# Optimization experiments

Hardware: AMD Instinct MI355X
Metric: run time of the kernel (lower is better)

Reference implementation:

```python
import jax, jax.numpy as jnp
import numpy as np

B, S, HID, NH, HD, NL = 2, 4096, 1024, 16, 64, 128
N_ITER = 6


def setup_inputs() -> dict:
    key = jax.random.key(0)
    ks = jax.random.split(key, 9)
    s = 0.02
    D = NH * HD
    return {
        "X": jax.random.normal(ks[0], (B, S, HID), jnp.float32),
        "mask": jnp.ones((B, S), jnp.float32),
        "Wq": jax.random.normal(ks[1], (HID, D), jnp.float32) * s,
        "bq": jnp.zeros((D,), jnp.float32),
        "Wk": jax.random.normal(ks[2], (HID, D), jnp.float32) * s,
        "bk": jnp.zeros((D,), jnp.float32),
        "Wv": jax.random.normal(ks[3], (HID, D), jnp.float32) * s,
        "bv": jnp.zeros((D,), jnp.float32),
        "Wo": jax.random.normal(ks[4], (D, HID), jnp.float32) * s,
        "bo": jnp.zeros((HID,), jnp.float32),
    }


def iterative_inv(mat, n_iter=N_ITER):
    # Newton-Schulz style pseudo-inverse iteration (Nystromformer 'original' init)
    I = jnp.eye(mat.shape[-1], dtype=mat.dtype)
    K = mat
    V = K.swapaxes(-1, -2) / jnp.max(jnp.sum(K, axis=-2))
    for _ in range(n_iter):
        KV = K @ V
        V = 0.25 * V @ (13.0 * I - KV @ (15.0 * I - KV @ (7.0 * I - KV)))
    return V


def nystrom_core(Q, K, V, mask):
    # Q,K,V: [B,NH,S,HD], mask: [B,S]
    scale = 1.0 / np.sqrt(np.sqrt(HD))  # 1/d^(1/4) applied to both Q and K
    m = mask[:, None, :, None]
    Q = Q * m * scale
    K = K * m * scale
    seg = S // NL
    # landmarks: mean over contiguous segments -> [B,NH,NL,HD]
    Ql = Q.reshape(B, NH, NL, seg, HD).mean(axis=-2)
    Kl = K.reshape(B, NH, NL, seg, HD).mean(axis=-2)
    k1 = jax.nn.softmax(jnp.einsum('bhsd,bhld->bhsl', Q, Kl), axis=-1)   # [B,NH,S,NL]
    k2 = jax.nn.softmax(jnp.einsum('bhld,bhmd->bhlm', Ql, Kl), axis=-1)  # [B,NH,NL,NL]
    k3 = jax.nn.softmax(
        jnp.einsum('bhld,bhsd->bhls', Ql, K) - 1e9 * (1.0 - mask[:, None, None, :]),
        axis=-1)                                                          # [B,NH,NL,S]
    return k1 @ iterative_inv(k2) @ (k3 @ V)                              # [B,NH,S,HD]


def reference(X, mask, Wq, bq, Wk, bk, Wv, bv, Wo, bo):
    def split(Y):  # [B,S,NH*HD] -> [B,NH,S,HD]
        return Y.reshape(B, S, NH, HD).transpose(0, 2, 1, 3)
    Q = split(X @ Wq + bq)
    K = split(X @ Wk + bk)
    V = split(X @ Wv + bv)
    attn = nystrom_core(Q.astype(jnp.float32), K.astype(jnp.float32),
                        V.astype(jnp.float32), mask.astype(jnp.float32))
    out = attn.transpose(0, 2, 1, 3).reshape(B, S, NH * HD)
    return out @ Wo + bo
```

## Files before the change

### kernel.cpp

```cpp
#include <hip/hip_runtime.h>
#include <math.h>

constexpr int cB = 2, cS = 4096, cHID = 1024, cNH = 16, cHD = 64, cNL = 128, cSEG = 32, cD = 1024, cBH = 32;
constexpr float cSCALE = 0.35355339059327373f;

typedef _Float16 f16x8 __attribute__((ext_vector_type(8)));
typedef float f32x4 __attribute__((ext_vector_type(4)));

__device__ inline void gload_lds16(const void* g, void* l) {
    __builtin_amdgcn_global_load_lds(
        (const __attribute__((address_space(1))) void*)g,
        (__attribute__((address_space(3))) void*)l, 16, 0, 0);
}

__global__ __launch_bounds__(256) void wcast_t(
    const float* __restrict__ Wq, const float* __restrict__ Wk,
    const float* __restrict__ Wv, const float* __restrict__ Wo,
    _Float16* __restrict__ WqT, _Float16* __restrict__ WkT,
    _Float16* __restrict__ WvT, _Float16* __restrict__ WoT)
{
    __shared__ float tile[32][33];
    const int wsel = blockIdx.z;
    const float* W = (wsel == 0) ? Wq : (wsel == 1 ? Wk : (wsel == 2 ? Wv : Wo));
    _Float16* WT   = (wsel == 0) ? WqT : (wsel == 1 ? WkT : (wsel == 2 ? WvT : WoT));
    const int n0 = blockIdx.x * 32, k0 = blockIdx.y * 32;
    const int t = threadIdx.x;
    const int r = t >> 3, c = (t & 7) * 4;
    float4 v = *reinterpret_cast<const float4*>(W + (size_t)(k0 + r) * cD + n0 + c);
    tile[r][c] = v.x; tile[r][c + 1] = v.y; tile[r][c + 2] = v.z; tile[r][c + 3] = v.w;
    __syncthreads();
    union { _Float16 h[4]; ushort4 u; } p;
    p.h[0] = (_Float16)tile[c + 0][r]; p.h[1] = (_Float16)tile[c + 1][r];
    p.h[2] = (_Float16)tile[c + 2][r]; p.h[3] = (_Float16)tile[c + 3][r];
    *reinterpret_cast<ushort4*>(WT + (size_t)(n0 + r) * cHID + k0 + c) = p.u;
}

__global__ __launch_bounds__(64) void xm_kernel(
    const float* __restrict__ X, const float* __restrict__ mask,
    float* __restrict__ Xm, float* __restrict__ mbar, _Float16* __restrict__ Xh)
{
    const int bl = blockIdx.x;
    const int q  = blockIdx.y;
    const int b = bl >> 7, l = bl & 127;
    const int c = q * 256 + threadIdx.x * 4;
    float4 a = {0.f, 0.f, 0.f, 0.f};
    float msum = 0.f;
    for (int j = 0; j < cSEG; ++j) {
        float m = mask[b * cS + l * cSEG + j];
        size_t roff = ((size_t)(b * cS + l * cSEG + j)) * cHID + c;
        float4 x = *reinterpret_cast<const float4*>(X + roff);
        union { _Float16 h[4]; ushort4 u; } p;
        p.h[0] = (_Float16)x.x; p.h[1] = (_Float16)x.y;
        p.h[2] = (_Float16)x.z; p.h[3] = (_Float16)x.w;
        *reinterpret_cast<ushort4*>(Xh + roff) = p.u;
        a.x += m * x.x; a.y += m * x.y; a.z += m * x.z; a.w += m * x.w;
        msum += m;
    }
    const float inv = 1.0f / cSEG;
    a.x *= inv; a.y *= inv; a.z *= inv; a.w *= inv;
    *reinterpret_cast<float4*>(Xm + (size_t)bl * cHID + c) = a;
    if (q == 0 && threadIdx.x == 0) mbar[bl] = msum * inv;
}

__global__ __launch_bounds__(256) void qkv_gemm_f16(
    const _Float16* __restrict__ Xh, const float* __restrict__ mask,
    const _Float16* __restrict__ WqT, const _Float16* __restrict__ WkT, const _Float16* __restrict__ WvT,
    const float* __restrict__ bq, const float* __restrict__ bk, const float* __restrict__ bv,
    _Float16* __restrict__ Qh, _Float16* __restrict__ Kh, _Float16* __restrict__ Vh)
{
    __shared__ __align__(16) _Float16 As[128 * 64];
    __shared__ __align__(16) _Float16 Bs[128 * 64];
    const int wsel = blockIdx.z;
    const _Float16* WT = (wsel == 0) ? WqT : (wsel == 1 ? WkT : WvT);
    const float* bias  = (wsel == 0) ? bq  : (wsel == 1 ? bk  : bv);
    _Float16* Y        = (wsel == 0) ? Qh  : (wsel == 1 ? Kh  : Vh);
    const int orig = blockIdx.x;
    const int xcd = orig & 7, idx = orig >> 3;
    const int n0 = (idx & 7) * 128;
    const int m0 = (xcd * 8 + (idx >> 3)) * 128;
    const int t = threadIdx.x;
    const int wave = t >> 6, lane = t & 63;
    const int wm = (wave >> 1) * 64, wn = (wave & 1) * 64;
    const int quad = lane >> 4, l15 = lane & 15;
    const int srow = wave * 8 + (lane >> 3);
    const int scol = ((lane & 7) ^ (lane >> 3)) * 8;

    f32x4 acc[4][4];
#pragma unroll
    for (int i = 0; i < 4; ++i)
#pragma unroll
        for (int j = 0; j < 4; ++j) acc[i][j] = (f32x4){0.f, 0.f, 0.f, 0.f};

    for (int k0 = 0; k0 < cHID; k0 += 64) {
        const _Float16* aSrc = Xh + (size_t)(m0 + srow) * cHID + k0 + scol;
        const _Float16* bSrc = WT + (size_t)(n0 + srow) * cHID + k0 + scol;
#pragma unroll
        for (int i = 0; i < 4; ++i) {
            gload_lds16(aSrc + (size_t)(i * 32) * cHID, &As[(wave * 8 + i * 32) * 64]);
            gload_lds16(bSrc + (size_t)(i * 32) * cHID, &Bs[(wave * 8 + i * 32) * 64]);
        }
        __syncthreads();
        f16x8 af[2][4], bf[2][4];
#pragma unroll
        for (int kh = 0; kh < 2; ++kh) {
            const int cg = ((kh * 4 + quad) ^ (l15 & 7)) * 8;
#pragma unroll
            for (int mt = 0; mt < 4; ++mt)
                af[kh][mt] = *reinterpret_cast<const f16x8*>(&As[(wm + mt * 16 + l15) * 64 + cg]);
#pragma unroll
            for (int nt = 0; nt < 4; ++nt)
                bf[kh][nt] = *reinterpret_cast<const f16x8*>(&Bs[(wn + nt * 16 + l15) * 64 + cg]);
        }
#pragma unroll
        for (int kh = 0; kh < 2; ++kh)
#pragma unroll
            for (int mt = 0; mt < 4; ++mt)
#pragma unroll
                for (int nt = 0; nt < 4; ++nt)
                    acc[mt][nt] = __builtin_amdgcn_mfma_f32_16x16x32_f16(af[kh][mt], bf[kh][nt], acc[mt][nt], 0, 0, 0);
        __syncthreads();
    }
#pragma unroll
    for (int mt = 0; mt < 4; ++mt) {
#pragma unroll
        for (int r = 0; r < 4; ++r) {
            int R = m0 + wm + mt * 16 + quad * 4 + r;
            int b = R >> 12, s = R & (cS - 1);
            float msc = (wsel < 2) ? mask[b * cS + s] * cSCALE : 1.0f;
#pragma unroll
            for (int nt = 0; nt < 4; ++nt) {
                int Cc = n0 + wn + nt * 16 + l15;
                int h = Cc >> 6, d = Cc & 63;
                float val = (acc[mt][nt][r] + bias[Cc]) * msc;
                Y[((size_t)(b * cNH + h) * cS + s) * cHD + d] = (_Float16)val;
            }
        }
    }
}

__global__ __launch_bounds__(256) void out_gemm_f16(
    const _Float16* __restrict__ Ah, const _Float16* __restrict__ WT,
    const float* __restrict__ bias, float* __restrict__ Y)
{
    __shared__ __align__(16) _Float16 As[128 * 64];
    __shared__ __align__(16) _Float16 Bs[128 * 64];
    const int orig = blockIdx.x;
    const int xcd = orig & 7, idx = orig >> 3;
    const int n0 = (idx & 7) * 128;
    const int m0 = (xcd * 8 + (idx >> 3)) * 128;
    const int t = threadIdx.x;
    const int wave = t >> 6, lane = t & 63;
    const int wm = (wave >> 1) * 64, wn = (wave & 1) * 64;
    const int quad = lane >> 4, l15 = lane & 15;
    const int srow = wave * 8 + (lane >> 3);
    const int scol = ((lane & 7) ^ (lane >> 3)) * 8;

    f32x4 acc[4][4];
#pragma unroll
    for (int i = 0; i < 4; ++i)
#pragma unroll
        for (int j = 0; j < 4; ++j) acc[i][j] = (f32x4){0.f, 0.f, 0.f, 0.f};

    for (int k0 = 0; k0 < cD; k0 += 64) {
        const _Float16* aSrc = Ah + (size_t)(m0 + srow) * cD + k0 + scol;
        const _Float16* bSrc = WT + (size_t)(n0 + srow) * cD + k0 + scol;
#pragma unroll
        for (int i = 0; i < 4; ++i) {
            gload_lds16(aSrc + (size_t)(i * 32) * cD, &As[(wave * 8 + i * 32) * 64]);
            gload_lds16(bSrc + (size_t)(i * 32) * cD, &Bs[(wave * 8 + i * 32) * 64]);
        }
        __syncthreads();
        f16x8 af[2][4], bf[2][4];
#pragma unroll
        for (int kh = 0; kh < 2; ++kh) {
            const int cg = ((kh * 4 + quad) ^ (l15 & 7)) * 8;
#pragma unroll
            for (int mt = 0; mt < 4; ++mt)
                af[kh][mt] = *reinterpret_cast<const f16x8*>(&As[(wm + mt * 16 + l15) * 64 + cg]);
#pragma unroll
            for (int nt = 0; nt < 4; ++nt)
                bf[kh][nt] = *reinterpret_cast<const f16x8*>(&Bs[(wn + nt * 16 + l15) * 64 + cg]);
        }
#pragma unroll
        for (int kh = 0; kh < 2; ++kh)
#pragma unroll
            for (int mt = 0; mt < 4; ++mt)
#pragma unroll
                for (int nt = 0; nt < 4; ++nt)
                    acc[mt][nt] = __builtin_amdgcn_mfma_f32_16x16x32_f16(af[kh][mt], bf[kh][nt], acc[mt][nt], 0, 0, 0);
        __syncthreads();
    }
#pragma unroll
    for (int mt = 0; mt < 4; ++mt) {
#pragma unroll
        for (int r = 0; r < 4; ++r) {
            int R = m0 + wm + mt * 16 + quad * 4 + r;
#pragma unroll
            for (int nt = 0; nt < 4; ++nt) {
                int Cc = n0 + wn + nt * 16 + l15;
                Y[(size_t)R * cHID + Cc] = acc[mt][nt][r] + bias[Cc];
            }
        }
    }
}

__global__ __launch_bounds__(256) void lgemm(
    const float* __restrict__ Xm, const float* __restrict__ mbar,
    const float* __restrict__ Wq, const float* __restrict__ bq,
    const float* __restrict__ Wk, const float* __restrict__ bk,
    float* __restrict__ Ql, float* __restrict__ Kl,
    _Float16* __restrict__ Qlh, _Float16* __restrict__ Klh)
{
    __shared__ __align__(16) float As[16][68];
    __shared__ __align__(16) float Bs[16][68];
    const int tid = threadIdx.x;
    const int wsel = blockIdx.z;
    const float* W    = wsel ? Wk : Wq;
    const float* bias = wsel ? bk : bq;
    float* Yl         = wsel ? Kl : Ql;
    _Float16* Ylh     = wsel ? Klh : Qlh;
// ... 40 lines not shown
}

__global__ __launch_bounds__(128) void k2_softmax(
    const float* __restrict__ Ql, const float* __restrict__ Kl, float* __restrict__ k2)
{
    __shared__ __align__(16) float qrow[64];
    __shared__ float red[128];
    int bh = blockIdx.x >> 7, i = blockIdx.x & 127;
    int j = threadIdx.x;
    if (j < 64) qrow[j] = Ql[(bh * cNL + i) * cHD + j];
    __syncthreads();
    const float4* q4  = reinterpret_cast<const float4*>(qrow);
    const float4* kl4 = reinterpret_cast<const float4*>(Kl + (bh * cNL + j) * cHD);
    float dot = 0.f;
#pragma unroll
    for (int u = 0; u < 16; ++u) {
        float4 a = q4[u], b = kl4[u];
        dot += a.x * b.x + a.y * b.y + a.z * b.z + a.w * b.w;
    }
    red[j] = dot; __syncthreads();
    for (int off = 64; off > 0; off >>= 1) { if (j < off) red[j] = fmaxf(red[j], red[j + off]); __syncthreads(); }
    float m = red[0]; __syncthreads();
    float e = expf(dot - m);
    red[j] = e; __syncthreads();
    for (int off = 64; off > 0; off >>= 1) { if (j < off) red[j] += red[j + off]; __syncthreads(); }
    k2[(bh * cNL + i) * cNL + j] = e / red[0];
}

__global__ __launch_bounds__(128) void colsum_max(const float* __restrict__ k2, int* __restrict__ cmax)
{
    __shared__ float red[128];
    int bh = blockIdx.x, j = threadIdx.x;
    float s = 0.f;
    for (int i = 0; i < cNL; ++i) s += k2[(bh * cNL + i) * cNL + j];
    red[j] = s; __syncthreads();
    for (int off = 64; off > 0; off >>= 1) { if (j < off) red[j] = fmaxf(red[j], red[j + off]); __syncthreads(); }
    if (j == 0) atomicMax(cmax, __float_as_int(red[0]));
}

__device__ inline void split2(float v, _Float16& h, _Float16& l) {
    h = (_Float16)v;
    l = (_Float16)(v - (float)h);
}
__device__ inline unsigned short f16bits(_Float16 h) { return __builtin_bit_cast(unsigned short, h); }

#define NYS_MFMA(a, b, c) __builtin_amdgcn_mfma_f32_16x16x32_f16((a), (b), (c), 0, 0, 0)

#define NYS_PRELOAD(PH, PL, LH, LL)                                                     \
    {                                                                                   \
        _Pragma("unroll")                                                               \
        for (int mt_ = 0; mt_ < 4; ++mt_) {                                             \
            const int rowL_ = wr * 64 + mt_ * 16 + l15;                                 \
            _Pragma("unroll")                                                           \
            for (int k0_ = 0; k0_ < 4; ++k0_) {                                         \
                LH[mt_][k0_] = *reinterpret_cast<const f16x8*>(&PH[rowL_ * 136 + k0_ * 32 + quad * 8]); \
                LL[mt_][k0_] = *reinterpret_cast<const f16x8*>(&PL[rowL_ * 136 + k0_ * 32 + quad * 8]); \
            }                                                                           \
        }                                                                               \
    }

#define NYS_PRODUCT(PH, PL, LH, LL)                                                     \
    {                                                                                   \
        _Pragma("unroll")                                                               \
        for (int mt_ = 0; mt_ < 4; ++mt_)                                               \
            _Pragma("unroll")                                                           \
            for (int nt_ = 0; nt_ < 2; ++nt_) acc[mt_][nt_] = (f32x4){0.f, 0.f, 0.f, 0.f}; \
        _Pragma("unroll")                                                               \
        for (int nt_ = 0; nt_ < 2; ++nt_) {                                             \
            _Pragma("unroll")                                                           \
            for (int k0_ = 0; k0_ < 4; ++k0_) {                                         \
                const int boff_ = (wcb + nt_ * 16) * 136 + k0_ * 32 + quad * 8;         \
                f16x8 bh_ = *reinterpret_cast<const f16x8*>(&PH[boff_]);                \
                f16x8 bl_ = *reinterpret_cast<const f16x8*>(&PL[boff_]);                \
                _Pragma("unroll")                                                       \
                for (int mt_ = 0; mt_ < 4; ++mt_) {                                     \
                    acc[mt_][nt_] = NYS_MFMA(LH[mt_][k0_], bh_, acc[mt_][nt_]);         \
                    acc[mt_][nt_] = NYS_MFMA(LL[mt_][k0_], bh_, acc[mt_][nt_]);         \
                    acc[mt_][nt_] = NYS_MFMA(LH[mt_][k0_], bl_, acc[mt_][nt_]);         \
                }                                                                       \
            }                                                                           \
        }                                                                               \
    }

__global__ __launch_bounds__(512, 2) void nys_k3v(
    const float* __restrict__ k2, const int* __restrict__ cmax,
    float* __restrict__ Mg0, float* __restrict__ Mg1,
    const _Float16* __restrict__ Qlh, const _Float16* __restrict__ Kh,
    const _Float16* __restrict__ VTh, const float* __restrict__ mask,
    float* __restrict__ Opart, float* __restrict__ mpart, float* __restrict__ spart)
{
    __shared__ __align__(16) _Float16 SMEM[4 * 128 * 136];

    if (blockIdx.x < 32) {
        _Float16* Ahi_s = SMEM;
        _Float16* Alo_s = SMEM + 128 * 136;
        _Float16* Whi_s = SMEM + 2 * 128 * 136;
        _Float16* Wlo_s = SMEM + 3 * 128 * 136;
        const int bh = blockIdx.x;
        const int t = threadIdx.x;
        const int wave = t >> 6, lane = t & 63;
        const int wr = wave >> 2, wc = wave & 3;
        const int quad = lane >> 4, l15 = lane & 15;
        const int wcb = wc * 32 + l15;
        const float* Kg = k2 + (size_t)bh * 16384;
        float* Mg0b = Mg0 + (size_t)bh * 16384;
        float* Mg1b = Mg1 + (size_t)bh * 16384;
        const float sc = sqrtf(1.0f / __int_as_float(*cmax));

        {
            const int row = t >> 2, c0 = (t & 3) * 32;
            const float* src = Kg + row * 128 + c0;
            _Float16* dh = &Whi_s[row * 136 + c0];
            _Float16* dl = &Wlo_s[row * 136 + c0];
#pragma unroll
            for (int u = 0; u < 32; u += 4) {
                float4 v = *reinterpret_cast<const float4*>(src + u);
                ushort4 ph, pl; _Float16 h, l;
                split2(v.x * sc, h, l); ph.x = f16bits(h); pl.x = f16bits(l);
                split2(v.y * sc, h, l); ph.y = f16bits(h); pl.y = f16bits(l);
                split2(v.z * sc, h, l); ph.z = f16bits(h); pl.z = f16bits(l);
                split2(v.w * sc, h, l); ph.w = f16bits(h); pl.w = f16bits(l);
                *reinterpret_cast<ushort4*>(dh + u) = ph;
                *reinterpret_cast<ushort4*>(dl + u) = pl;
            }
        }
        __syncthreads();

        f32x4 acc[4][2];
        f16x8 Fh[4][4], Fl[4][4];

        NYS_PRELOAD(Whi_s, Wlo_s, Fh, Fl);
        NYS_PRODUCT(Whi_s, Wlo_s, Fh, Fl);
#pragma unroll
        for (int mt = 0; mt < 4; ++mt)
#pragma unroll
            for (int nt = 0; nt < 2; ++nt) {
                const int col = wcb + nt * 16;
                const int rb  = wr * 64 + mt * 16 + quad * 4;
                ushort4 ph, pl;
#pragma unroll
                for (int r = 0; r < 4; ++r) {
                    _Float16 h, l; split2(acc[mt][nt][r], h, l);
                    ((unsigned short*)&ph)[r] = f16bits(h);
                    ((unsigned short*)&pl)[r] = f16bits(l);
                }
                *reinterpret_cast<ushort4*>(&Ahi_s[col * 136 + rb]) = ph;
                *reinterpret_cast<ushort4*>(&Alo_s[col * 136 + rb]) = pl;
            }
        __syncthreads();

        for (int it = 0; it < 6; ++it) {
            NYS_PRELOAD(Ahi_s, Alo_s, Fh, Fl);
            NYS_PRODUCT(Ahi_s, Alo_s, Fh, Fl);
#pragma unroll
            for (int mt = 0; mt < 4; ++mt)
#pragma unroll
                for (int nt = 0; nt < 2; ++nt) {
                    const int col = wcb + nt * 16;
                    const int rb  = wr * 64 + mt * 16 + quad * 4;
                    ushort4 ah = *reinterpret_cast<const ushort4*>(&Ahi_s[col * 136 + rb]);
                    ushort4 al = *reinterpret_cast<const ushort4*>(&Alo_s[col * 136 + rb]);
                    ushort4 ph, pl;
#pragma unroll
                    for (int r = 0; r < 4; ++r) {
                        float av = (float)__builtin_bit_cast(_Float16, ((unsigned short*)&ah)[r])
                                 + (float)__builtin_bit_cast(_Float16, ((unsigned short*)&al)[r]);
                        float v = ((rb + r) == col ? 15.0f : 0.0f) - 7.0f * av + acc[mt][nt][r];
                        _Float16 h, l; split2(v, h, l);
                        ((unsigned short*)&ph)[r] = f16bits(h);
                        ((unsigned short*)&pl)[r] = f16bits(l);
                    }
                    *reinterpret_cast<ushort4*>(&Whi_s[col * 136 + rb]) = ph;
// ... 11 lines not shown
                    ushort4 ph, pl; float4 mv;
#pragma unroll
                    for (int r = 0; r < 4; ++r) {
                        float v = ((rb + r) == col ? 13.0f : 0.0f) - acc[mt][nt][r];
                        _Float16 h, l; split2(v, h, l);
                        ((unsigned short*)&ph)[r] = f16bits(h);
                        ((unsigned short*)&pl)[r] = f16bits(l);
                        ((float*)&mv)[r] = 0.25f * v;
                    }
                    *reinterpret_cast<ushort4*>(&Whi_s[col * 136 + rb]) = ph;
                    *reinterpret_cast<ushort4*>(&Wlo_s[col * 136 + rb]) = pl;
                    if (it == 0)
                        *reinterpret_cast<float4*>(&Mg0b[col * 128 + rb]) = mv;
                }
            __syncthreads();
            NYS_PRODUCT(Whi_s, Wlo_s, Fh, Fl);
#pragma unroll
            for (int mt = 0; mt < 4; ++mt)
#pragma unroll
                for (int nt = 0; nt < 2; ++nt) {
                    const int col = wcb + nt * 16;
                    const int rb  = wr * 64 + mt * 16 + quad * 4;
                    ushort4 ph, pl;
#pragma unroll
                    for (int r = 0; r < 4; ++r) {
                        _Float16 h, l; split2(0.25f * acc[mt][nt][r], h, l);
                        ((unsigned short*)&ph)[r] = f16bits(h);
                        ((unsigned short*)&pl)[r] = f16bits(l);
                    }
                    *reinterpret_cast<ushort4*>(&Ahi_s[col * 136 + rb]) = ph;
                    *reinterpret_cast<ushort4*>(&Alo_s[col * 136 + rb]) = pl;
                }
            if (it >= 1) {
                const float* Mr = (it & 1) ? Mg0b : Mg1b;
                float*       Mw = (it & 1) ? Mg1b : Mg0b;
#pragma unroll
                for (int mt = 0; mt < 4; ++mt)
#pragma unroll
                    for (int nt = 0; nt < 2; ++nt) acc[mt][nt] = (f32x4){0.f, 0.f, 0.f, 0.f};
#pragma unroll
                for (int k0 = 0; k0 < 4; ++k0) {
                    f16x8 Mh[4], Ml[4];
#pragma unroll
                    for (int mt = 0; mt < 4; ++mt) {
                        const int rowL = wr * 64 + mt * 16 + l15;
                        const float* src = Mr + rowL * 128 + k0 * 32 + quad * 8;
                        float4 v0 = *reinterpret_cast<const float4*>(src);
                        float4 v1 = *reinterpret_cast<const float4*>(src + 4);
                        union { f16x8 v; _Float16 e[8]; } hh, ll;
                        split2(v0.x, hh.e[0], ll.e[0]); split2(v0.y, hh.e[1], ll.e[1]);
                        split2(v0.z, hh.e[2], ll.e[2]); split2(v0.w, hh.e[3], ll.e[3]);
                        split2(v1.x, hh.e[4], ll.e[4]); split2(v1.y, hh.e[5], ll.e[5]);
                        split2(v1.z, hh.e[6], ll.e[6]); split2(v1.w, hh.e[7], ll.e[7]);
                        Mh[mt] = hh.v; Ml[mt] = ll.v;
                    }
#pragma unroll
                    for (int nt = 0; nt < 2; ++nt) {
                        const int boff = (wcb + nt * 16) * 136 + k0 * 32 + quad * 8;
                        f16x8 bh_ = *reinterpret_cast<const f16x8*>(&Whi_s[boff]);
                        f16x8 bl_ = *reinterpret_cast<const f16x8*>(&Wlo_s[boff]);
#pragma unroll
                        for (int mt = 0; mt < 4; ++mt) {
                            acc[mt][nt] = NYS_MFMA(Mh[mt], bh_, acc[mt][nt]);
                            acc[mt][nt] = NYS_MFMA(Ml[mt], bh_, acc[mt][nt]);
                            acc[mt][nt] = NYS_MFMA(Mh[mt], bl_, acc[mt][nt]);
                        }
                    }
                }
#pragma unroll
                for (int mt = 0; mt < 4; ++mt)
#pragma unroll
                    for (int nt = 0; nt < 2; ++nt) {
                        const int col = wcb + nt * 16;
                        const int rb  = wr * 64 + mt * 16 + quad * 4;
                        float4 mv;
#pragma unroll
                        for (int r = 0; r < 4; ++r) ((float*)&mv)[r] = 0.25f * acc[mt][nt][r];
                        *reinterpret_cast<float4*>(&Mw[col * 128 + rb]) = mv;
                    }
            }
            __syncthreads();
        }
    } else {
        const int t = threadIdx.x;
        const int wave8 = t >> 6;
        const int wg = wave8 >> 2;
        const int wave = wave8 & 3;
        _Float16* Ps = SMEM + (size_t)wg * (128 * 72);
        const int zz = (blockIdx.x - 32) * 2 + wg;
        const int z = zz & 15, bh = zz >> 4;
        const int b = bh >> 4;
        const int sbase = z * 256;
        const int lane = t & 63;
        const int quad = lane >> 4, l15 = lane & 15;

        f16x8 aq[2][2];
        const _Float16* qlg = Qlh + (size_t)bh * cNL * cHD;
#pragma unroll
        for (int mt = 0; mt < 2; ++mt)
#pragma unroll
            for (int k0 = 0; k0 < 2; ++k0)
                aq[mt][k0] = *reinterpret_cast<const f16x8*>(
                    qlg + (size_t)(wave * 32 + mt * 16 + l15) * cHD + k0 * 32 + quad * 8);

        float mrun[2][4], srun[2][4];
        f32x4 accO[2][4];
#pragma unroll
        for (int mt = 0; mt < 2; ++mt)
#pragma unroll
            for (int r = 0; r < 4; ++r) { mrun[mt][r] = -1e30f; srun[mt][r] = 0.f; }
#pragma unroll
        for (int mt = 0; mt < 2; ++mt)
#pragma unroll
            for (int dt = 0; dt < 4; ++dt) accO[mt][dt] = (f32x4){0.f, 0.f, 0.f, 0.f};

        const _Float16* kg = Kh + (size_t)bh * cS * cHD;
        const _Float16* vg = VTh + (size_t)bh * cHD * cS;

        for (int step = 0; step < 4; ++step) {
            const int st = sbase + step * 64;
            f32x4 accS[2][4];
#pragma unroll
            for (int mt = 0; mt < 2; ++mt)
#pragma unroll
                for (int nt = 0; nt < 4; ++nt) accS[mt][nt] = (f32x4){0.f, 0.f, 0.f, 0.f};
#pragma unroll
            for (int k0 = 0; k0 < 2; ++k0)
#pragma unroll
                for (int nt = 0; nt < 4; ++nt) {
                    f16x8 bk = *reinterpret_cast<const f16x8*>(
                        kg + (size_t)(st + nt * 16 + l15) * cHD + k0 * 32 + quad * 8);
#pragma unroll
                    for (int mt = 0; mt < 2; ++mt)
                        accS[mt][nt] = __builtin_amdgcn_mfma_f32_16x16x32_f16(aq[mt][k0], bk, accS[mt][nt], 0, 0, 0);
                }
#pragma unroll
            for (int nt = 0; nt < 4; ++nt) {
                float pen = 1e9f * (1.0f - mask[b * cS + st + nt * 16 + l15]);
#pragma unroll
                for (int mt = 0; mt < 2; ++mt)
#pragma unroll
                    for (int r = 0; r < 4; ++r) accS[mt][nt][r] -= pen;
            }
#pragma unroll
            for (int mt = 0; mt < 2; ++mt) {
#pragma unroll
                for (int r = 0; r < 4; ++r) {
                    float tmax = fmaxf(fmaxf(accS[mt][0][r], accS[mt][1][r]),
                                       fmaxf(accS[mt][2][r], accS[mt][3][r]));
#pragma unroll
                    for (int w = 1; w < 16; w <<= 1) tmax = fmaxf(tmax, __shfl_xor(tmax, w, 16));
                    float mnew = fmaxf(mrun[mt][r], tmax);
                    float alpha = __expf(mrun[mt][r] - mnew);
                    float ts = 0.f;
#pragma unroll
                    for (int nt = 0; nt < 4; ++nt) {
                        float e = __expf(accS[mt][nt][r] - mnew);
                        accS[mt][nt][r] = e; ts += e;
                    }
#pragma unroll
                    for (int w = 1; w < 16; w <<= 1) ts += __shfl_xor(ts, w, 16);
                    srun[mt][r] = srun[mt][r] * alpha + ts;
                    mrun[mt][r] = mnew;
#pragma unroll
                    for (int dt = 0; dt < 4; ++dt) accO[mt][dt][r] *= alpha;
                }
            }
#pragma unroll
            for (int mt = 0; mt < 2; ++mt)
#pragma unroll
                for (int nt = 0; nt < 4; ++nt)
#pragma unroll
                    for (int r = 0; r < 4; ++r)
                        Ps[(wave * 32 + mt * 16 + quad * 4 + r) * 72 + nt * 16 + l15] =
                            (_Float16)accS[mt][nt][r];
#pragma unroll
            for (int k0 = 0; k0 < 2; ++k0) {
                f16x8 ap[2];
#pragma unroll
                for (int mt = 0; mt < 2; ++mt)
                    ap[mt] = *reinterpret_cast<const f16x8*>(
                        &Ps[(wave * 32 + mt * 16 + l15) * 72 + k0 * 32 + quad * 8]);
#pragma unroll
                for (int dt = 0; dt < 4; ++dt) {
                    f16x8 bv = *reinterpret_cast<const f16x8*>(
                        vg + (size_t)(dt * 16 + l15) * cS + st + k0 * 32 + quad * 8);
#pragma unroll
                    for (int mt = 0; mt < 2; ++mt)
                        accO[mt][dt] = __builtin_amdgcn_mfma_f32_16x16x32_f16(ap[mt], bv, accO[mt][dt], 0, 0, 0);
                }
            }
        }
        const int rowbase = bh * cNL + wave * 32;
#pragma unroll
        for (int mt = 0; mt < 2; ++mt)
#pragma unroll
            for (int dt = 0; dt < 4; ++dt)
#pragma unroll
                for (int r = 0; r < 4; ++r)
                    Opart[(size_t)(z * 4096 + rowbase + mt * 16 + quad * 4 + r) * cHD + dt * 16 + l15] =
                        accO[mt][dt][r];
        if (l15 == 0) {
#pragma unroll
            for (int mt = 0; mt < 2; ++mt)
#pragma unroll
                for (int r = 0; r < 4; ++r) {
                    int prow = z * 4096 + rowbase + mt * 16 + quad * 4 + r;
                    mpart[prow] = mrun[mt][r];
                    spart[prow] = srun[mt][r];
                }
        }
    }
}

__global__ __launch_bounds__(256) void vtrans(const _Float16* __restrict__ Vh, _Float16* __restrict__ VTh)
{
    __shared__ ushort T[64][72];
    const int s0 = blockIdx.x * 64, bh = blockIdx.y;
    const int t = threadIdx.x;
    const _Float16* vb = Vh + ((size_t)bh * cS + s0) * cHD;
#pragma unroll
    for (int i = 0; i < 2; ++i) {
        int idx = t + i * 256;
        int row = idx >> 3, c8 = idx & 7;
        f16x8 v = *reinterpret_cast<const f16x8*>(vb + (size_t)row * cHD + c8 * 8);
#pragma unroll
        for (int j = 0; j < 8; ++j) T[row][c8 * 8 + j] = ((ushort*)&v)[j];
    }
    __syncthreads();
    _Float16* vt = VTh + (size_t)bh * cHD * cS;
#pragma unroll
    for (int i = 0; i < 2; ++i) {
        int idx = t + i * 256;
        int d = idx >> 3, s8 = idx & 7;
        f16x8 o;
#pragma unroll
        for (int j = 0; j < 8; ++j) ((ushort*)&o)[j] = T[s8 * 8 + j][d];
        *reinterpret_cast<f16x8*>(vt + (size_t)d * cS + s0 + s8 * 8) = o;
    }
}

__global__ __launch_bounds__(256) void w2_matmul(
    const float* __restrict__ k2, const float* __restrict__ M6,
    const int* __restrict__ cmax,
    const float* __restrict__ Opart, const float* __restrict__ mpart,
    const float* __restrict__ spart,
    _Float16* __restrict__ W2T)
{
    __shared__ __align__(16) float CVs[128][68];
    __shared__ __align__(16) float Us[128][68];
    const int bh = blockIdx.x, t = threadIdx.x;
    const float invc = 1.0f / __int_as_float(*cmax);
    for (int it = 0; it < 32; ++it) {
        int idx = t + it * 256;
        int row = idx >> 6, d = idx & 63;
        int grow = bh * cNL + row;
        float mstar = -1e30f;
#pragma unroll
        for (int z = 0; z < 16; ++z) mstar = fmaxf(mstar, mpart[z * 4096 + grow]);
        float ssum = 0.f, acc = 0.f;
#pragma unroll
        for (int z = 0; z < 16; ++z) {
            float w = __expf(mpart[z * 4096 + grow] - mstar);
            ssum += w * spart[z * 4096 + grow];
            acc  += w * Opart[(size_t)(z * 4096 + grow) * cHD + d];
        }
        CVs[row][d] = acc / ssum;
    }
    __syncthreads();
    const float* Mg = M6 + (size_t)bh * 16384;
    {
        const int tx = t & 15, ty = t >> 4;
        float acc[8][4] = {};
        for (int k = 0; k < 128; ++k) {
            float4 b4 = *reinterpret_cast<const float4*>(&CVs[k][tx * 4]);
#pragma unroll
            for (int i = 0; i < 8; ++i) {
                float a = Mg[(ty * 8 + i) * 128 + k];
                acc[i][0] += a * b4.x; acc[i][1] += a * b4.y; acc[i][2] += a * b4.z; acc[i][3] += a * b4.w;
            }
        }
#pragma unroll
        for (int i = 0; i < 8; ++i)
#pragma unroll
            for (int j = 0; j < 4; ++j)
                Us[ty * 8 + i][tx * 4 + j] = acc[i][j];
    }
    __syncthreads();
    {
        const int l = t & 127, dg = (t >> 7) * 32;
        float acc2[32];
#pragma unroll
        for (int dd = 0; dd < 32; ++dd) acc2[dd] = 0.f;
        const float* kg = k2 + (size_t)bh * 16384;
        for (int j = 0; j < 128; ++j) {
            float kv = kg[j * 128 + l];
#pragma unroll
            for (int dd = 0; dd < 32; ++dd) acc2[dd] += kv * Us[j][dg + dd];
        }
        _Float16* wt = W2T + (size_t)bh * (cHD * cNL);
#pragma unroll
        for (int dd = 0; dd < 32; ++dd)
            wt[(size_t)(dg + dd) * cNL + l] = (_Float16)(acc2[dd] * invc);
    }
}

__global__ __launch_bounds__(256) void k1_mfma(
    const _Float16* __restrict__ Qh, const _Float16* __restrict__ Klh,
    const _Float16* __restrict__ W2T, _Float16* __restrict__ ctxh)
{
    __shared__ __align__(16) _Float16 Qs[64 * 72];
    __shared__ __align__(16) _Float16 Ps[64 * 136];
    const int s0 = blockIdx.x * 64, bh = blockIdx.y;
    const int b = bh >> 4, h = bh & 15;
    const int t = threadIdx.x;
    const int wave = t >> 6, lane = t & 63;
    const int quad = lane >> 4, l15 = lane & 15;

    {
        const _Float16* qg = Qh + ((size_t)bh * cS + s0) * cHD;
#pragma unroll
// ... 51 lines not shown
    f32x4 accO[4];
#pragma unroll
    for (int nt = 0; nt < 4; ++nt) accO[nt] = (f32x4){0.f, 0.f, 0.f, 0.f};
#pragma unroll
    for (int k0 = 0; k0 < 4; ++k0) {
        f16x8 ap = *reinterpret_cast<const f16x8*>(&Ps[(wave * 16 + l15) * 136 + k0 * 32 + quad * 8]);
#pragma unroll
        for (int nt = 0; nt < 4; ++nt) {
            f16x8 bw = *reinterpret_cast<const f16x8*>(wtg + (size_t)(nt * 16 + l15) * cNL + k0 * 32 + quad * 8);
            accO[nt] = __builtin_amdgcn_mfma_f32_16x16x32_f16(ap, bw, accO[nt], 0, 0, 0);
        }
    }
#pragma unroll
    for (int nt = 0; nt < 4; ++nt)
#pragma unroll
        for (int r = 0; r < 4; ++r) {
            int s = s0 + wave * 16 + quad * 4 + r;
            int d = nt * 16 + l15;
            ctxh[((size_t)(b * cS) + s) * cD + h * cHD + d] = (_Float16)accO[nt][r];
        }
}

extern "C" void kernel_launch(void* const* d_in, const int* in_sizes, int n_in,
                              void* d_out, int out_size, void* d_ws, size_t ws_size,
                              hipStream_t stream)
{
    const float* X    = (const float*)d_in[0];
    const float* mask = (const float*)d_in[1];
    const float* Wq   = (const float*)d_in[2];
    const float* bq   = (const float*)d_in[3];
    const float* Wk   = (const float*)d_in[4];
    const float* bk   = (const float*)d_in[5];
    const float* Wv   = (const float*)d_in[6];
    const float* bv   = (const float*)d_in[7];
    const float* Wo   = (const float*)d_in[8];
    const float* bo   = (const float*)d_in[9];
    float* out = (float*)d_out;

    float* ws = (float*)d_ws;
    size_t off = 0;
    const size_t szQKV = (size_t)cBH * cS * cHD;
    const size_t szL   = (size_t)cBH * cNL * cHD;
    const size_t szM   = (size_t)cBH * cNL * cNL;
    float* Qr   = ws + off; off += szQKV;
    float* Kr   = ws + off; off += szQKV;
    float* Vr   = ws + off; off += szQKV;
    _Float16* Xh  = (_Float16*)(ws + off); off += szQKV / 2;
    _Float16* WqT = (_Float16*)(ws + off); off += 524288;
    _Float16* WkT = (_Float16*)(ws + off); off += 524288;
    _Float16* WvT = (_Float16*)(ws + off); off += 524288;
    _Float16* WoT = (_Float16*)(ws + off); off += 524288;
    float* Xm   = ws + off; off += (size_t)cB * cNL * cHID;
    float* mbar = ws + off; off += 256;
    float* Ql  = ws + off; off += szL;
    float* Kl  = ws + off; off += szL;
    float* k2  = ws + off; off += szM;
    float* Mg0 = ws + off; off += szM;
    float* Mg1 = ws + off; off += szM;
    float* T1b = ws + off; off += szM;
    float* T2b = ws + off; off += szM;
    float* T3b = ws + off; off += szM;
    float* CV  = ws + off; off += szL;
    _Float16* Qlh  = (_Float16*)(ws + off); off += szL / 2;
    _Float16* Klh  = (_Float16*)(ws + off); off += szL / 2;
    _Float16* W2Th = (_Float16*)(ws + off); off += szL / 2;
    int*   cmax = (int*)(ws + off); off += 16;
    float* mpart = ws + off; off += 65536;
    float* spart = ws + off; off += 65536;

    _Float16* Qh   = (_Float16*)Qr;
    float*    Opart = Qr + szQKV / 2;
    _Float16* Kh   = (_Float16*)Kr;
    _Float16* ctxh = (_Float16*)(Kr + szQKV / 2);
    _Float16* Vh   = (_Float16*)Vr;
    _Float16* VTh  = (_Float16*)(Vr + szQKV / 2);

    (void)T1b; (void)T2b; (void)T3b; (void)CV;

    hipMemsetAsync(cmax, 0, sizeof(int), stream);

    wcast_t<<<dim3(32, 32, 4), 256, 0, stream>>>(Wq, Wk, Wv, Wo, WqT, WkT, WvT, WoT);
    xm_kernel<<<dim3(cB * cNL, 4), 64, 0, stream>>>(X, mask, Xm, mbar, Xh);

    qkv_gemm_f16<<<dim3(512, 1, 3), 256, 0, stream>>>(
        Xh, mask, WqT, WkT, WvT, bq, bk, bv, Qh, Kh, Vh);
    vtrans<<<dim3(cS / 64, cBH), 256, 0, stream>>>(Vh, VTh);
    lgemm<<<dim3(cD / 64, (cB * cNL) / 64, 2), 256, 0, stream>>>(Xm, mbar, Wq, bq, Wk, bk, Ql, Kl, Qlh, Klh);

    k2_softmax<<<cBH * cNL, 128, 0, stream>>>(Ql, Kl, k2);
    colsum_max<<<cBH, 128, 0, stream>>>(k2, cmax);

    nys_k3v<<<dim3(32 + 256), 512, 0, stream>>>(
        k2, cmax, Mg0, Mg1, Qlh, Kh, VTh, mask, Opart, mpart, spart);

    w2_matmul<<<cBH, 256, 0, stream>>>(k2, Mg1, cmax, Opart, mpart, spart, W2Th);
    k1_mfma<<<dim3(cS / 64, cBH), 256, 0, stream>>>(Qh, Klh, W2Th, ctxh);
    out_gemm_f16<<<dim3(512), 256, 0, stream>>>(ctxh, WoT, bo, out);
}
```

Before: 476.5 us.

## Co-schedule QKV projection GEMM with Newton-Schulz inverse in one launch

The QKV projection GEMM moves out of its own kernel and into the branch of the fused kernel that runs alongside the 32 iterative-inverse blocks. Each 512-thread block computes two 128x128 output tiles, one per 256-thread half. The k3·V streaming-softmax work, which used to share that kernel, becomes its own launch after the V transpose and stages the mask in LDS. The aim is to hide the latency-bound inverse iteration behind the bandwidth- and compute-heavy GEMM. The risk is that both halves of a block share __syncthreads, and the GEMM now runs at the lower occupancy of the larger block.

```diff
diff --git a/kernel.cpp b/kernel.cpp
--- a/kernel.cpp
+++ b/kernel.cpp
@@ -60,82 +60,6 @@
     a.x *= inv; a.y *= inv; a.z *= inv; a.w *= inv;
     *reinterpret_cast<float4*>(Xm + (size_t)bl * cHID + c) = a;
     if (q == 0 && threadIdx.x == 0) mbar[bl] = msum * inv;
-}
-
-__global__ __launch_bounds__(256) void qkv_gemm_f16(
-    const _Float16* __restrict__ Xh, const float* __restrict__ mask,
-    const _Float16* __restrict__ WqT, const _Float16* __restrict__ WkT, const _Float16* __restrict__ WvT,
-    const float* __restrict__ bq, const float* __restrict__ bk, const float* __restrict__ bv,
-    _Float16* __restrict__ Qh, _Float16* __restrict__ Kh, _Float16* __restrict__ Vh)
-{
-    __shared__ __align__(16) _Float16 As[128 * 64];
-    __shared__ __align__(16) _Float16 Bs[128 * 64];
-    const int wsel = blockIdx.z;
-    const _Float16* WT = (wsel == 0) ? WqT : (wsel == 1 ? WkT : WvT);
-    const float* bias  = (wsel == 0) ? bq  : (wsel == 1 ? bk  : bv);
-    _Float16* Y        = (wsel == 0) ? Qh  : (wsel == 1 ? Kh  : Vh);
-    const int orig = blockIdx.x;
-    const int xcd = orig & 7, idx = orig >> 3;
-    const int n0 = (idx & 7) * 128;
-    const int m0 = (xcd * 8 + (idx >> 3)) * 128;
-    const int t = threadIdx.x;
-    const int wave = t >> 6, lane = t & 63;
-    const int wm = (wave >> 1) * 64, wn = (wave & 1) * 64;
-    const int quad = lane >> 4, l15 = lane & 15;
-    const int srow = wave * 8 + (lane >> 3);
-    const int scol = ((lane & 7) ^ (lane >> 3)) * 8;
-
-    f32x4 acc[4][4];
-#pragma unroll
-    for (int i = 0; i < 4; ++i)
-#pragma unroll
-        for (int j = 0; j < 4; ++j) acc[i][j] = (f32x4){0.f, 0.f, 0.f, 0.f};
-
-    for (int k0 = 0; k0 < cHID; k0 += 64) {
-        const _Float16* aSrc = Xh + (size_t)(m0 + srow) * cHID + k0 + scol;
-        const _Float16* bSrc = WT + (size_t)(n0 + srow) * cHID + k0 + scol;
-#pragma unroll
-        for (int i = 0; i < 4; ++i) {
-            gload_lds16(aSrc + (size_t)(i * 32) * cHID, &As[(wave * 8 + i * 32) * 64]);
-            gload_lds16(bSrc + (size_t)(i * 32) * cHID, &Bs[(wave * 8 + i * 32) * 64]);
-        }
-        __syncthreads();
-        f16x8 af[2][4], bf[2][4];
-#pragma unroll
-        for (int kh = 0; kh < 2; ++kh) {
-            const int cg = ((kh * 4 + quad) ^ (l15 & 7)) * 8;
-#pragma unroll
-            for (int mt = 0; mt < 4; ++mt)
-                af[kh][mt] = *reinterpret_cast<const f16x8*>(&As[(wm + mt * 16 + l15) * 64 + cg]);
-#pragma unroll
-            for (int nt = 0; nt < 4; ++nt)
-                bf[kh][nt] = *reinterpret_cast<const f16x8*>(&Bs[(wn + nt * 16 + l15) * 64 + cg]);
-        }
-#pragma unroll
-        for (int kh = 0; kh < 2; ++kh)
-#pragma unroll
-            for (int mt = 0; mt < 4; ++mt)
-#pragma unroll
-                for (int nt = 0; nt < 4; ++nt)
-                    acc[mt][nt] = __builtin_amdgcn_mfma_f32_16x16x32_f16(af[kh][mt], bf[kh][nt], acc[mt][nt], 0, 0, 0);
-        __syncthreads();
-    }
-#pragma unroll
-    for (int mt = 0; mt < 4; ++mt) {
-#pragma unroll
-        for (int r = 0; r < 4; ++r) {
-            int R = m0 + wm + mt * 16 + quad * 4 + r;
-            int b = R >> 12, s = R & (cS - 1);
-            float msc = (wsel < 2) ? mask[b * cS + s] * cSCALE : 1.0f;
-#pragma unroll
-            for (int nt = 0; nt < 4; ++nt) {
-                int Cc = n0 + wn + nt * 16 + l15;
-                int h = Cc >> 6, d = Cc & 63;
-                float val = (acc[mt][nt][r] + bias[Cc]) * msc;
-                Y[((size_t)(b * cNH + h) * cS + s) * cHD + d] = (_Float16)val;
-            }
-        }
-    }
 }
 
 __global__ __launch_bounds__(256) void out_gemm_f16(
@@ -342,12 +266,13 @@
         }                                                                               \
     }
 
-__global__ __launch_bounds__(512, 2) void nys_k3v(
+__global__ __launch_bounds__(512, 2) void nys_qkv(
     const float* __restrict__ k2, const int* __restrict__ cmax,
     float* __restrict__ Mg0, float* __restrict__ Mg1,
-    const _Float16* __restrict__ Qlh, const _Float16* __restrict__ Kh,
-    const _Float16* __restrict__ VTh, const float* __restrict__ mask,
-    float* __restrict__ Opart, float* __restrict__ mpart, float* __restrict__ spart)
+    const _Float16* __restrict__ Xh, const float* __restrict__ mask,
+    const _Float16* __restrict__ WqT, const _Float16* __restrict__ WkT, const _Float16* __restrict__ WvT,
+    const float* __restrict__ bq, const float* __restrict__ bk, const float* __restrict__ bv,
+    _Float16* __restrict__ Qh, _Float16* __restrict__ Kh, _Float16* __restrict__ Vh)
 {
     __shared__ __align__(16) _Float16 SMEM[4 * 128 * 136];
 
@@ -525,133 +450,78 @@
             __syncthreads();
         }
     } else {
-        const int t = threadIdx.x;
-        const int wave8 = t >> 6;
-        const int wg = wave8 >> 2;
-        const int wave = wave8 & 3;
-        _Float16* Ps = SMEM + (size_t)wg * (128 * 72);
-        const int zz = (blockIdx.x - 32) * 2 + wg;
-        const int z = zz & 15, bh = zz >> 4;
-        const int b = bh >> 4;
-        const int sbase = z * 256;
-        const int lane = t & 63;
+        const int half = threadIdx.x >> 8;
+        const int t = threadIdx.x & 255;
+        _Float16* As = SMEM + (size_t)half * 16384;
+        _Float16* Bs = As + 8192;
+        const int r = blockIdx.x - 32;
+        const int wsel = r >> 8;
+        const int rr = r & 255;
+        const int xcd = rr & 7;
+        const int q = rr >> 3;
+        const int mtile = xcd * 8 + (q >> 2);
+        const int ntile = (q & 3) * 2 + half;
+        const int m0 = mtile * 128, n0 = ntile * 128;
+        const _Float16* WT = (wsel == 0) ? WqT : (wsel == 1 ? WkT : WvT);
+        const float* bias  = (wsel == 0) ? bq  : (wsel == 1 ? bk  : bv);
+        _Float16* Y        = (wsel == 0) ? Qh  : (wsel == 1 ? Kh  : Vh);
+
+        const int wave = t >> 6, lane = t & 63;
+        const int wm = (wave >> 1) * 64, wn = (wave & 1) * 64;
         const int quad = lane >> 4, l15 = lane & 15;
-
-        f16x8 aq[2][2];
-        const _Float16* qlg = Qlh + (size_t)bh * cNL * cHD;
-#pragma unroll
-        for (int mt = 0; mt < 2; ++mt)
-#pragma unroll
-            for (int k0 = 0; k0 < 2; ++k0)
-                aq[mt][k0] = *reinterpret_cast<const f16x8*>(
-                    qlg + (size_t)(wave * 32 + mt * 16 + l15) * cHD + k0 * 32 + quad * 8);
-
-        float mrun[2][4], srun[2][4];
-        f32x4 accO[2][4];
-#pragma unroll
-        for (int mt = 0; mt < 2; ++mt)
-#pragma unroll
-            for (int r = 0; r < 4; ++r) { mrun[mt][r] = -1e30f; srun[mt][r] = 0.f; }
-#pragma unroll
-        for (int mt = 0; mt < 2; ++mt)
-#pragma unroll
-            for (int dt = 0; dt < 4; ++dt) accO[mt][dt] = (f32x4){0.f, 0.f, 0.f, 0.f};
-
-        const _Float16* kg = Kh + (size_t)bh * cS * cHD;
-        const _Float16* vg = VTh + (size_t)bh * cHD * cS;
-
-        for (int step = 0; step < 4; ++step) {
-            const int st = sbase + step * 64;
-            f32x4 accS[2][4];
-#pragma unroll
-            for (int mt = 0; mt < 2; ++mt)
-#pragma unroll
-                for (int nt = 0; nt < 4; ++nt) accS[mt][nt] = (f32x4){0.f, 0.f, 0.f, 0.f};
-#pragma unroll
-            for (int k0 = 0; k0 < 2; ++k0)
+        const int srow = wave * 8 + (lane >> 3);
+        const int scol = ((lane & 7) ^ (lane >> 3)) * 8;
+
+        f32x4 acc[4][4];
+#pragma unroll
+        for (int i = 0; i < 4; ++i)
+#pragma unroll
+            for (int j = 0; j < 4; ++j) acc[i][j] = (f32x4){0.f, 0.f, 0.f, 0.f};
+
+        for (int k0 = 0; k0 < cHID; k0 += 64) {
+            const _Float16* aSrc = Xh + (size_t)(m0 + srow) * cHID + k0 + scol;
+            const _Float16* bSrc = WT + (size_t)(n0 + srow) * cHID + k0 + scol;
+#pragma unroll
+            for (int i = 0; i < 4; ++i) {
+                gload_lds16(aSrc + (size_t)(i * 32) * cHID, &As[(wave * 8 + i * 32) * 64]);
+                gload_lds16(bSrc + (size_t)(i * 32) * cHID, &Bs[(wave * 8 + i * 32) * 64]);
+            }
+            __syncthreads();
+            f16x8 af[2][4], bf[2][4];
+#pragma unroll
+            for (int kh = 0; kh < 2; ++kh) {
+                const int cg = ((kh * 4 + quad) ^ (l15 & 7)) * 8;
+#pragma unroll
+                for (int mt = 0; mt < 4; ++mt)
+                    af[kh][mt] = *reinterpret_cast<const f16x8*>(&As[(wm + mt * 16 + l15) * 64 + cg]);
+#pragma unroll
+                for (int nt = 0; nt < 4; ++nt)
+                    bf[kh][nt] = *reinterpret_cast<const f16x8*>(&Bs[(wn + nt * 16 + l15) * 64 + cg]);
+            }
+#pragma unroll
+            for (int kh = 0; kh < 2; ++kh)
+#pragma unroll
+                for (int mt = 0; mt < 4; ++mt)
+#pragma unroll
+                    for (int nt = 0; nt < 4; ++nt)
+                        acc[mt][nt] = __builtin_amdgcn_mfma_f32_16x16x32_f16(af[kh][mt], bf[kh][nt], acc[mt][nt], 0, 0, 0);
+            __syncthreads();
+        }
+#pragma unroll
+        for (int mt = 0; mt < 4; ++mt) {
+#pragma unroll
+            for (int rI = 0; rI < 4; ++rI) {
+                int R = m0 + wm + mt * 16 + quad * 4 + rI;
+                int b = R >> 12, s = R & (cS - 1);
+                float msc = (wsel < 2) ? mask[b * cS + s] * cSCALE : 1.0f;
 #pragma unroll
                 for (int nt = 0; nt < 4; ++nt) {
-                    f16x8 bk = *reinterpret_cast<const f16x8*>(
-                        kg + (size_t)(st + nt * 16 + l15) * cHD + k0 * 32 + quad * 8);
-#pragma unroll
-                    for (int mt = 0; mt < 2; ++mt)
-                        accS[mt][nt] = __builtin_amdgcn_mfma_f32_16x16x32_f16(aq[mt][k0], bk, accS[mt][nt], 0, 0, 0);
+                    int Cc = n0 + wn + nt * 16 + l15;
+                    int h = Cc >> 6, d = Cc & 63;
+                    float val = (acc[mt][nt][rI] + bias[Cc]) * msc;
+                    Y[((size_t)(b * cNH + h) * cS + s) * cHD + d] = (_Float16)val;
                 }
-#pragma unroll
-            for (int nt = 0; nt < 4; ++nt) {
-                float pen = 1e9f * (1.0f - mask[b * cS + st + nt * 16 + l15]);
-#pragma unroll
-                for (int mt = 0; mt < 2; ++mt)
-#pragma unroll
-                    for (int r = 0; r < 4; ++r) accS[mt][nt][r] -= pen;
-            }
-#pragma unroll
-            for (int mt = 0; mt < 2; ++mt) {
-#pragma unroll
-                for (int r = 0; r < 4; ++r) {
-                    float tmax = fmaxf(fmaxf(accS[mt][0][r], accS[mt][1][r]),
-                                       fmaxf(accS[mt][2][r], accS[mt][3][r]));
-#pragma unroll
-                    for (int w = 1; w < 16; w <<= 1) tmax = fmaxf(tmax, __shfl_xor(tmax, w, 16));
-                    float mnew = fmaxf(mrun[mt][r], tmax);
-                    float alpha = __expf(mrun[mt][r] - mnew);
-                    float ts = 0.f;
-#pragma unroll
-                    for (int nt = 0; nt < 4; ++nt) {
-                        float e = __expf(accS[mt][nt][r] - mnew);
-                        accS[mt][nt][r] = e; ts += e;
-                    }
-#pragma unroll
-                    for (int w = 1; w < 16; w <<= 1) ts += __shfl_xor(ts, w, 16);
-                    srun[mt][r] = srun[mt][r] * alpha + ts;
-                    mrun[mt][r] = mnew;
-#pragma unroll
-                    for (int dt = 0; dt < 4; ++dt) accO[mt][dt][r] *= alpha;
-                }
-            }
-#pragma unroll
-            for (int mt = 0; mt < 2; ++mt)
-#pragma unroll
-                for (int nt = 0; nt < 4; ++nt)
-#pragma unroll
-                    for (int r = 0; r < 4; ++r)
-                        Ps[(wave * 32 + mt * 16 + quad * 4 + r) * 72 + nt * 16 + l15] =
-                            (_Float16)accS[mt][nt][r];
-#pragma unroll
-            for (int k0 = 0; k0 < 2; ++k0) {
-                f16x8 ap[2];
-#pragma unroll
-                for (int mt = 0; mt < 2; ++mt)
-                    ap[mt] = *reinterpret_cast<const f16x8*>(
-                        &Ps[(wave * 32 + mt * 16 + l15) * 72 + k0 * 32 + quad * 8]);
-#pragma unroll
-                for (int dt = 0; dt < 4; ++dt) {
-                    f16x8 bv = *reinterpret_cast<const f16x8*>(
-                        vg + (size_t)(dt * 16 + l15) * cS + st + k0 * 32 + quad * 8);
-#pragma unroll
-                    for (int mt = 0; mt < 2; ++mt)
-                        accO[mt][dt] = __builtin_amdgcn_mfma_f32_16x16x32_f16(ap[mt], bv, accO[mt][dt], 0, 0, 0);
-                }
-            }
-        }
-        const int rowbase = bh * cNL + wave * 32;
-#pragma unroll
-        for (int mt = 0; mt < 2; ++mt)
-#pragma unroll
-            for (int dt = 0; dt < 4; ++dt)
-#pragma unroll
-                for (int r = 0; r < 4; ++r)
-                    Opart[(size_t)(z * 4096 + rowbase + mt * 16 + quad * 4 + r) * cHD + dt * 16 + l15] =
-                        accO[mt][dt][r];
-        if (l15 == 0) {
-#pragma unroll
-            for (int mt = 0; mt < 2; ++mt)
-#pragma unroll
-                for (int r = 0; r < 4; ++r) {
-                    int prow = z * 4096 + rowbase + mt * 16 + quad * 4 + r;
-                    mpart[prow] = mrun[mt][r];
-                    spart[prow] = srun[mt][r];
-                }
+            }
         }
     }
 }
@@ -680,6 +550,142 @@
 #pragma unroll
         for (int j = 0; j < 8; ++j) ((ushort*)&o)[j] = T[s8 * 8 + j][d];
         *reinterpret_cast<f16x8*>(vt + (size_t)d * cS + s0 + s8 * 8) = o;
+    }
+}
+
+__global__ __launch_bounds__(256) void k3v_mfma(
+    const _Float16* __restrict__ Qlh, const _Float16* __restrict__ Kh,
+    const _Float16* __restrict__ VTh, const float* __restrict__ mask,
+    float* __restrict__ Opart, float* __restrict__ mpart, float* __restrict__ spart)
+{
+    __shared__ __align__(16) _Float16 Ps[128 * 72];
+    __shared__ float msk[256];
+    const int z = blockIdx.x, bh = blockIdx.y;
+    const int b = bh >> 4;
+    const int sbase = z * 256;
+    const int t = threadIdx.x;
+    const int wave = t >> 6, lane = t & 63;
+    const int quad = lane >> 4, l15 = lane & 15;
+
+    msk[t] = mask[b * cS + sbase + t];
+
+    f16x8 aq[2][2];
+    const _Float16* qlg = Qlh + (size_t)bh * cNL * cHD;
+#pragma unroll
+    for (int mt = 0; mt < 2; ++mt)
+#pragma unroll
+        for (int k0 = 0; k0 < 2; ++k0)
+            aq[mt][k0] = *reinterpret_cast<const f16x8*>(
+                qlg + (size_t)(wave * 32 + mt * 16 + l15) * cHD + k0 * 32 + quad * 8);
+
+    float mrun[2][4], srun[2][4];
+    f32x4 accO[2][4];
+#pragma unroll
+    for (int mt = 0; mt < 2; ++mt)
+#pragma unroll
+        for (int r = 0; r < 4; ++r) { mrun[mt][r] = -1e30f; srun[mt][r] = 0.f; }
+#pragma unroll
+    for (int mt = 0; mt < 2; ++mt)
+#pragma unroll
+        for (int dt = 0; dt < 4; ++dt) accO[mt][dt] = (f32x4){0.f, 0.f, 0.f, 0.f};
+
+    __syncthreads();
+
+    const _Float16* kg = Kh + (size_t)bh * cS * cHD;
+    const _Float16* vg = VTh + (size_t)bh * cHD * cS;
+
+    for (int step = 0; step < 4; ++step) {
+        const int st = sbase + step * 64;
+        f32x4 accS[2][4];
+#pragma unroll
+        for (int mt = 0; mt < 2; ++mt)
+#pragma unroll
+            for (int nt = 0; nt < 4; ++nt) accS[mt][nt] = (f32x4){0.f, 0.f, 0.f, 0.f};
+#pragma unroll
+        for (int k0 = 0; k0 < 2; ++k0)
+#pragma unroll
+            for (int nt = 0; nt < 4; ++nt) {
+                f16x8 bk = *reinterpret_cast<const f16x8*>(
+                    kg + (size_t)(st + nt * 16 + l15) * cHD + k0 * 32 + quad * 8);
+#pragma unroll
+                for (int mt = 0; mt < 2; ++mt)
+                    accS[mt][nt] = __builtin_amdgcn_mfma_f32_16x16x32_f16(aq[mt][k0], bk, accS[mt][nt], 0, 0, 0);
+            }
+#pragma unroll
+        for (int nt = 0; nt < 4; ++nt) {
+            float pen = 1e9f * (1.0f - msk[step * 64 + nt * 16 + l15]);
+#pragma unroll
+            for (int mt = 0; mt < 2; ++mt)
+#pragma unroll
+                for (int r = 0; r < 4; ++r) accS[mt][nt][r] -= pen;
+        }
+#pragma unroll
+        for (int mt = 0; mt < 2; ++mt) {
+#pragma unroll
+            for (int r = 0; r < 4; ++r) {
+                float tmax = fmaxf(fmaxf(accS[mt][0][r], accS[mt][1][r]),
+                                   fmaxf(accS[mt][2][r], accS[mt][3][r]));
+#pragma unroll
+                for (int w = 1; w < 16; w <<= 1) tmax = fmaxf(tmax, __shfl_xor(tmax, w, 16));
+                float mnew = fmaxf(mrun[mt][r], tmax);
+                float alpha = __expf(mrun[mt][r] - mnew);
+                float ts = 0.f;
+#pragma unroll
+                for (int nt = 0; nt < 4; ++nt) {
+                    float e = __expf(accS[mt][nt][r] - mnew);
+                    accS[mt][nt][r] = e; ts += e;
+                }
+#pragma unroll
+                for (int w = 1; w < 16; w <<= 1) ts += __shfl_xor(ts, w, 16);
+                srun[mt][r] = srun[mt][r] * alpha + ts;
+                mrun[mt][r] = mnew;
+#pragma unroll
+                for (int dt = 0; dt < 4; ++dt) accO[mt][dt][r] *= alpha;
+            }
+        }
+#pragma unroll
+        for (int mt = 0; mt < 2; ++mt)
+#pragma unroll
+            for (int nt = 0; nt < 4; ++nt)
+#pragma unroll
+                for (int r = 0; r < 4; ++r)
+                    Ps[(wave * 32 + mt * 16 + quad * 4 + r) * 72 + nt * 16 + l15] =
+                        (_Float16)accS[mt][nt][r];
+#pragma unroll
+        for (int k0 = 0; k0 < 2; ++k0) {
+            f16x8 ap[2];
+#pragma unroll
+            for (int mt = 0; mt < 2; ++mt)
+                ap[mt] = *reinterpret_cast<const f16x8*>(
+                    &Ps[(wave * 32 + mt * 16 + l15) * 72 + k0 * 32 + quad * 8]);
+#pragma unroll
+            for (int dt = 0; dt < 4; ++dt) {
+                f16x8 bv = *reinterpret_cast<const f16x8*>(
+                    vg + (size_t)(dt * 16 + l15) * cS + st + k0 * 32 + quad * 8);
+#pragma unroll
+                for (int mt = 0; mt < 2; ++mt)
+                    accO[mt][dt] = __builtin_amdgcn_mfma_f32_16x16x32_f16(ap[mt], bv, accO[mt][dt], 0, 0, 0);
+            }
+        }
+    }
+    const int rowbase = bh * cNL + wave * 32;
+#pragma unroll
+    for (int mt = 0; mt < 2; ++mt)
+#pragma unroll
+        for (int dt = 0; dt < 4; ++dt)
+#pragma unroll
+            for (int r = 0; r < 4; ++r)
+                Opart[(size_t)(z * 4096 + rowbase + mt * 16 + quad * 4 + r) * cHD + dt * 16 + l15] =
+                    accO[mt][dt][r];
+    if (l15 == 0) {
+#pragma unroll
+        for (int mt = 0; mt < 2; ++mt)
+#pragma unroll
+            for (int r = 0; r < 4; ++r) {
+                int prow = z * 4096 + rowbase + mt * 16 + quad * 4 + r;
+                mpart[prow] = mrun[mt][r];
+                spart[prow] = srun[mt][r];
+            }
     }
 }
 
@@ -897,16 +903,16 @@
     wcast_t<<<dim3(32, 32, 4), 256, 0, stream>>>(Wq, Wk, Wv, Wo, WqT, WkT, WvT, WoT);
     xm_kernel<<<dim3(cB * cNL, 4), 64, 0, stream>>>(X, mask, Xm, mbar, Xh);
 
-    qkv_gemm_f16<<<dim3(512, 1, 3), 256, 0, stream>>>(
-        Xh, mask, WqT, WkT, WvT, bq, bk, bv, Qh, Kh, Vh);
-    vtrans<<<dim3(cS / 64, cBH), 256, 0, stream>>>(Vh, VTh);
     lgemm<<<dim3(cD / 64, (cB * cNL) / 64, 2), 256, 0, stream>>>(Xm, mbar, Wq, bq, Wk, bk, Ql, Kl, Qlh, Klh);
-
     k2_softmax<<<cBH * cNL, 128, 0, stream>>>(Ql, Kl, k2);
     colsum_max<<<cBH, 128, 0, stream>>>(k2, cmax);
 
-    nys_k3v<<<dim3(32 + 256), 512, 0, stream>>>(
-        k2, cmax, Mg0, Mg1, Qlh, Kh, VTh, mask, Opart, mpart, spart);
+    nys_qkv<<<dim3(32 + 768), 512, 0, stream>>>(
+        k2, cmax, Mg0, Mg1,
+        Xh, mask, WqT, WkT, WvT, bq, bk, bv, Qh, Kh, Vh);
+
+    vtrans<<<dim3(cS / 64, cBH), 256, 0, stream>>>(Vh, VTh);
+    k3v_mfma<<<dim3(16, cBH), 256, 0, stream>>>(Qlh, Kh, VTh, mask, Opart, mpart, spart);
 
     w2_matmul<<<cBH, 256, 0, stream>>>(k2, Mg1, cmax, Opart, mpart, spart, W2Th);
     k1_mfma<<<dim3(cS / 64, cBH), 256, 0, stream>>>(Qh, Klh, W2Th, ctxh);
```

New measurement: 451.3 us. -5.3%, faster.
